# Kernel optimization log

Measured on AMD Instinct MI355X. Metric: run time of the kernel, lower is better.

## Reference

```python
import math
import jax, jax.numpy as jnp
import numpy as np

K_KDE = 50
K_RIPS = 16
SCALE = 30.0
DESTNUM = 10
THRESHOLD = 1.0  # hardcoded in topograd_loss
N, D = 8192, 64


def _knn(x, k):
    """Brute-force k-NN with squared L2 distances (faiss IndexFlatL2 semantics,
    self included as nearest neighbour). Returns (sq_dists[N,k], idxs[N,k]),
    neighbours sorted by increasing distance."""
    sq = jnp.sum(x * x, axis=1)
    d = sq[:, None] + sq[None, :] - 2.0 * (x @ x.T)  # [N,N]
    neg, idx = jax.lax.top_k(-d, k)
    return -neg, idx


def _cluster(density, rips_idxs, threshold):
    """Union-find re-implementation of the numba `cluster` routine.
    Iterates points from high density (index N-1) to low; each point joins the
    entry of its highest-index upward neighbour; other upward neighbours'
    entries are merged if their persistence is below threshold, and every
    cross-entry comparison emits a persistence pair (entry_idx, ref_idx).
    Returns the raw pers_pairs array (without the [-1,-1] sentinel rows)."""
    n = density.shape[0]
    parent = np.arange(n)
    name = np.arange(n)  # name[root] = entry id (a point index)

    def find(i):
        root = i
        while parent[root] != root:
            root = parent[root]
        while parent[i] != root:  # path compression
            parent[i], i = root, parent[i]
        return root

    pairs = []
    for i in range(n - 2, -1, -1):
        nbr = rips_idxs[i]
        us = nbr[nbr > i]  # upward (denser, already-processed) neighbours
        if us.size == 0:
            continue  # point i forms its own singleton entry
        e_up = name[find(int(us.max()))]
        parent[find(i)] = find(e_up)  # append i to entry e_up
        for j in us:
            ei = name[find(int(j))]
            if ei != e_up:
                pairs.append((ei, i))
                if density[ei] - density[i] < threshold:
                    parent[find(ei)] = find(e_up)  # merge entry ei into e_up
    return np.asarray(pairs, dtype=np.int64).reshape(-1, 2)


def _pd_pairs(pairs, n):
    """For each unique entry id in pairs[:,0], keep (entry_id, max ref idx)."""
    maxref = np.full(n, -1, dtype=np.int64)
    np.maximum.at(maxref, pairs[:, 0], pairs[:, 1])
    uniq = np.unique(pairs[:, 0])
    return np.stack([uniq, maxref[uniq]], axis=1)


def setup_inputs() -> dict:
    key = jax.random.key(0)
    x = jax.random.normal(key, (N, D), dtype=jnp.float32)
    return {"x": x}


def reference(x):
    # --- KNN kernel density estimate (differentiable) ---
    vals, _ = _knn(x, K_KDE)
    res = jnp.sum(jnp.exp(-vals / SCALE), axis=1) / (K_KDE * SCALE)
    dens = res / jnp.max(res)
    # --- sort by ascending density ---
    sorted_idxs = jnp.argsort(dens)
    dens_s = dens[sorted_idxs]
    x_s = x[sorted_idxs]
    # --- delta-Rips graph on sorted points ---
    _, rips_idxs = _knn(x_s, K_RIPS)
    # --- persistence clustering (non-differentiable, host) ---
    pairs = _cluster(np.asarray(dens_s), np.asarray(rips_idxs), THRESHOLD)
    pd = jnp.asarray(_pd_pairs(pairs, x.shape[0]))  # [P,2] int64
    # --- topological loss ---
    oripd = dens_s[pd]  # [P,2] (birth, death) densities
    sidx = jnp.argsort(oripd[:, 0] - oripd[:, 1])  # ascending persistence
    changepairs = pd[sidx[:-DESTNUM]]
    nochangepairs = pd[sidx[-DESTNUM:-1]]
    dest = jax.lax.stop_gradient(oripd[sidx[-1]])  # torch.as_tensor detaches
    pd11 = dens_s[changepairs]
    weakdist = jnp.sum(pd11[:, 0] - pd11[:, 1]) / math.sqrt(2.0)
    strongdist = jnp.sum(jnp.linalg.norm(dens_s[nochangepairs] - dest, axis=1))
    return weakdist + strongdist
```

## Files before the change

kernel.cpp:

```cpp
#include <hip/hip_runtime.h>
#include <stdint.h>

#define NN 8192
#define DD 64

using bf16x8 = __attribute__((ext_vector_type(8))) short;
using f32x4  = __attribute__((ext_vector_type(4))) float;

__device__ __forceinline__ unsigned short f2bf(float f){
  unsigned u = __float_as_uint(f);
  return (unsigned short)((u + 0x7FFFu + ((u >> 16) & 1u)) >> 16);
}

__global__ __launch_bounds__(256) void k_pre(const float* __restrict__ x, float* __restrict__ xT,
                                             float* __restrict__ sq, int do_tr,
                                             uint4* __restrict__ xfrag, int do_frag){
  __shared__ float tile[64*65];
  const int tid = threadIdx.x;
  const int b = blockIdx.x;
  for (int k = 0; k < 4; ++k){
    const int idx4 = tid + k*256;
    const float4 v = ((const float4*)(x + (size_t)b*4096))[idx4];
    const int row = idx4 >> 4, d0 = (idx4 & 15) * 4;
    tile[row*65 + d0 + 0] = v.x;
    tile[row*65 + d0 + 1] = v.y;
    tile[row*65 + d0 + 2] = v.z;
    tile[row*65 + d0 + 3] = v.w;
  }
  __syncthreads();
  if (do_tr){
    const int jj = tid & 15;
    const int dq = tid >> 4;
    for (int k = 0; k < 4; ++k){
      const int d = dq + 16*k;
      float4 o;
      o.x = tile[(jj*4+0)*65 + d];
      o.y = tile[(jj*4+1)*65 + d];
      o.z = tile[(jj*4+2)*65 + d];
      o.w = tile[(jj*4+3)*65 + d];
      ((float4*)xT)[(size_t)d*2048 + b*16 + jj] = o;
    }
  }
  if (do_frag){
    for (int ch = tid; ch < 512; ch += 256){
      const int c  = ch & 15;
      const int q  = (ch >> 4) & 3;
      const int m  = (ch >> 6) & 1;
      const int gl = ch >> 7;
      const float* sp = tile + (gl*16 + c)*65 + m*32 + q*8;
      unsigned short h[8];
#pragma unroll
      for (int i2 = 0; i2 < 8; ++i2) h[i2] = f2bf(sp[i2]);
      uint4 o;
      o.x = (unsigned)h[0] | ((unsigned)h[1] << 16);
      o.y = (unsigned)h[2] | ((unsigned)h[3] << 16);
      o.z = (unsigned)h[4] | ((unsigned)h[5] << 16);
      o.w = (unsigned)h[6] | ((unsigned)h[7] << 16);
      xfrag[(size_t)b*512 + ch] = o;
    }
  }
  if (tid < 64){
    float acc = 0.f;
    const float* rp = tile + tid*65;
    for (int d = 0; d < 64; ++d) acc = fmaf(rp[d], rp[d], acc);
    sq[b*64 + tid] = acc;
  }
}

template<bool XT>
__device__ __forceinline__ void dists_1024(const float* __restrict__ x, const float* __restrict__ xT,
                                           const float* __restrict__ xi, int jbase, int tid,
                                           float acc[8][4]){
#pragma unroll
  for (int r = 0; r < 8; ++r)
#pragma unroll
    for (int q = 0; q < 4; ++q) acc[r][q] = 0.f;
  const int j0 = jbase + tid*4;
  for (int dq = 0; dq < 16; ++dq){
    float4 vj[4];
    if (XT){
#pragma unroll
      for (int s = 0; s < 4; ++s)
        vj[s] = ((const float4*)xT)[(size_t)(dq*4+s)*2048 + (j0 >> 2)];
    } else {
#pragma unroll
      for (int s = 0; s < 4; ++s){
        const int d = dq*4 + s;
        vj[s].x = x[(size_t)(j0+0)*64 + d];
        vj[s].y = x[(size_t)(j0+1)*64 + d];
        vj[s].z = x[(size_t)(j0+2)*64 + d];
        vj[s].w = x[(size_t)(j0+3)*64 + d];
      }
    }
#pragma unroll
    for (int r = 0; r < 8; ++r){
      const float4 wv = ((const float4*)(xi + r*64))[dq];
      acc[r][0] = fmaf(vj[0].x, wv.x, acc[r][0]);
      acc[r][1] = fmaf(vj[0].y, wv.x, acc[r][1]);
      acc[r][2] = fmaf(vj[0].z, wv.x, acc[r][2]);
      acc[r][3] = fmaf(vj[0].w, wv.x, acc[r][3]);
      acc[r][0] = fmaf(vj[1].x, wv.y, acc[r][0]);
      acc[r][1] = fmaf(vj[1].y, wv.y, acc[r][1]);
      acc[r][2] = fmaf(vj[1].z, wv.y, acc[r][2]);
      acc[r][3] = fmaf(vj[1].w, wv.y, acc[r][3]);
      acc[r][0] = fmaf(vj[2].x, wv.z, acc[r][0]);
      acc[r][1] = fmaf(vj[2].y, wv.z, acc[r][1]);
      acc[r][2] = fmaf(vj[2].z, wv.z, acc[r][2]);
      acc[r][3] = fmaf(vj[2].w, wv.z, acc[r][3]);
      acc[r][0] = fmaf(vj[3].x, wv.w, acc[r][0]);
      acc[r][1] = fmaf(vj[3].y, wv.w, acc[r][1]);
      acc[r][2] = fmaf(vj[3].z, wv.w, acc[r][2]);
      acc[r][3] = fmaf(vj[3].w, wv.w, acc[r][3]);
    }
  }
}

template<bool XT>
__global__ __launch_bounds__(256) void k_samp(const float* __restrict__ x, const float* __restrict__ xT,
                                              const float* __restrict__ sq, float* __restrict__ tub){
  __shared__ __align__(16) float xi[8*64];
  __shared__ float sqi_s[8];
  __shared__ __align__(16) float samp[8*1024];
  const int tid = threadIdx.x;
  const int i0 = blockIdx.x * 8;
  for (int t = tid; t < 8*64; t += 256) xi[t] = x[(size_t)i0*64 + t];
  if (tid < 8) sqi_s[tid] = sq[i0+tid];
  __syncthreads();
  float sqir[8];
#pragma unroll
  for (int r = 0; r < 8; ++r) sqir[r] = sqi_s[r];

  const int w0 = (blockIdx.x * 1024) & 8191;
  float acc[8][4];
  dists_1024<XT>(x, xT, xi, w0, tid, acc);
  float sqj[4];
#pragma unroll
  for (int q = 0; q < 4; ++q) sqj[q] = sq[w0 + tid*4 + q];
#pragma unroll
  for (int r = 0; r < 8; ++r)
#pragma unroll
    for (int q = 0; q < 4; ++q)
      samp[r*1024 + tid*4 + q] = (sqir[r] + sqj[q]) - 2.f*acc[r][q];
  __syncthreads();
  const int wv = tid >> 6, lane = tid & 63;
  for (int rr = 0; rr < 2; ++rr){
    const int r = wv + rr*4;
    float v[16];
#pragma unroll
    for (int k2 = 0; k2 < 16; ++k2) v[k2] = samp[r*1024 + lane + 64*k2];
    unsigned lo = 0u, hi = 0x7F800001u;
    while (hi - lo > 1u){
      const unsigned mid = (lo + hi) >> 1;
      const float pf = __uint_as_float(mid);
      int c = 0;
#pragma unroll
      for (int k2 = 0; k2 < 16; ++k2) c += (v[k2] < pf) ? 1 : 0;
#pragma unroll
      for (int off = 32; off; off >>= 1) c += __shfl_xor(c, off);
      if (c >= 32) hi = mid; else lo = mid;
    }
    if (lane == 0) tub[i0 + r] = __uint_as_float(hi);
  }
}

__global__ __launch_bounds__(256) void k_filt(const float* __restrict__ x, const float* __restrict__ sq,
                                              const float* __restrict__ tub,
                                              const uint4* __restrict__ xfrag,
                                              unsigned char* __restrict__ nib){
  const int tid = threadIdx.x;
  const int l   = tid & 63;
  const int w   = tid >> 6;
  const int qh  = l >> 4;
  const int c16 = l & 15;
  const int i0  = blockIdx.x * 8;

  bf16x8 a0, a1;
#pragma unroll
  for (int i2 = 0; i2 < 8; ++i2){ a0[i2] = 0; a1[i2] = 0; }
  if (c16 < 8){
    const float* ap = x + (size_t)(i0 + c16)*64 + qh*8;
#pragma unroll
    for (int i2 = 0; i2 < 8; ++i2){
      a0[i2] = (short)f2bf(ap[i2]);
      a1[i2] = (short)f2bf(ap[i2 + 32]);
    }
  }
  float thr2[4];
#pragma unroll
  for (int rg = 0; rg < 4; ++rg){
    int row = qh*4 + rg; row = (row < 8) ? row : 0;
    thr2[rg] = tub[i0 + row] + 2.0f - sq[i0 + row];
  }

  const bf16x8* bfp = (const bf16x8*)xfrag + (size_t)w*128 + l;
  const float*  sqp = sq + w*16 + c16;
  unsigned char* nb = nib + (size_t)blockIdx.x*8192 + w*16 + c16;

  bf16x8 A0 = bfp[0],   A1 = bfp[64];     float SA = sqp[0];
  bf16x8 B0 = bfp[512], B1 = bfp[512+64]; float SB = sqp[64];
  for (int it = 0; it < 128; it += 2){
    const int n2 = (it+2 < 128) ? it+2 : 126;
    const int n3 = (it+3 < 128) ? it+3 : 127;
    bf16x8 N0 = bfp[(size_t)n2*512], N1 = bfp[(size_t)n2*512 + 64];
    bf16x8 M0 = bfp[(size_t)n3*512], M1 = bfp[(size_t)n3*512 + 64];
    const float SN = sqp[n2*64], SM = sqp[n3*64];
    {
      f32x4 acc = {0.f, 0.f, 0.f, 0.f};
      acc = __builtin_amdgcn_mfma_f32_16x16x32_bf16(a0, A0, acc, 0, 0, 0);
      acc = __builtin_amdgcn_mfma_f32_16x16x32_bf16(a1, A1, acc, 0, 0, 0);
      unsigned m4 = 0u;
      m4 |= (fmaf(-2.f, acc[0], SA) < thr2[0]) ? 1u : 0u;
      m4 |= (fmaf(-2.f, acc[1], SA) < thr2[1]) ? 2u : 0u;
      m4 |= (fmaf(-2.f, acc[2], SA) < thr2[2]) ? 4u : 0u;
      m4 |= (fmaf(-2.f, acc[3], SA) < thr2[3]) ? 8u : 0u;
      const unsigned pm = (unsigned)__shfl((int)m4, (l + 16) & 63);
      if (l < 16) nb[it*64] = (unsigned char)(m4 | (pm << 4));
    }
    {
      f32x4 acc = {0.f, 0.f, 0.f, 0.f};
      acc = __builtin_amdgcn_mfma_f32_16x16x32_bf16(a0, B0, acc, 0, 0, 0);
      acc = __builtin_amdgcn_mfma_f32_16x16x32_bf16(a1, B1, acc, 0, 0, 0);
      unsigned m4 = 0u;
      m4 |= (fmaf(-2.f, acc[0], SB) < thr2[0]) ? 1u : 0u;
      m4 |= (fmaf(-2.f, acc[1], SB) < thr2[1]) ? 2u : 0u;
      m4 |= (fmaf(-2.f, acc[2], SB) < thr2[2]) ? 4u : 0u;
      m4 |= (fmaf(-2.f, acc[3], SB) < thr2[3]) ? 8u : 0u;
      const unsigned pm = (unsigned)__shfl((int)m4, (l + 16) & 63);
      if (l < 16) nb[(it+1)*64] = (unsigned char)(m4 | (pm << 4));
    }
    A0 = N0; A1 = N1; SA = SN;
    B0 = M0; B1 = M1; SB = SM;
  }
}

__global__ __launch_bounds__(256) void k_csort(const float* __restrict__ x, const float* __restrict__ sq,
                                               const float* __restrict__ tub,
                                               const unsigned char* __restrict__ nib,
                                               float* __restrict__ res, unsigned short* __restrict__ nn16){
  __shared__ __align__(16) float xi[8*68];
  __shared__ float sqi_s[8];
  __shared__ float tubs[8];
  __shared__ __align__(16) unsigned long long cand[8*512];
  __shared__ unsigned ccnt[8];
  const int tid = threadIdx.x;
  const int i0 = blockIdx.x * 8;
  for (int t = tid; t < 8*64; t += 256) xi[(t >> 6)*68 + (t & 63)] = x[(size_t)i0*64 + t];
  if (tid < 8){ sqi_s[tid] = sq[i0+tid]; tubs[tid] = tub[i0+tid]; ccnt[tid] = 0u; }
  for (int t = tid; t < 8*512; t += 256) cand[t] = ~0ULL;
  __syncthreads();

  const uint4* nb4 = (const uint4*)(nib + (size_t)blockIdx.x*8192);
  for (int u = tid; u < 512; u += 256){
    const uint4 v4 = nb4[u];
    unsigned wds[4] = {v4.x, v4.y, v4.z, v4.w};
#pragma unroll
    for (int ww = 0; ww < 4; ++ww){
      unsigned wvv = wds[ww];
      while (wvv){
        const int bit = __builtin_ctz(wvv);
        wvv &= wvv - 1u;
        const int byte = bit >> 3;
        const int r = bit & 7;
        const int j = u*16 + ww*4 + byte;
        const float* xj = x + (size_t)j*64;
        const float* xr = xi + r*68;
        float acc = 0.f;
#pragma unroll
        for (int d4 = 0; d4 < 16; ++d4){
          const float4 vj4 = ((const float4*)xj)[d4];
          const float4 wi4 = ((const float4*)xr)[d4];
          acc = fmaf(vj4.x, wi4.x, acc);
          acc = fmaf(vj4.y, wi4.y, acc);
          acc = fmaf(vj4.z, wi4.z, acc);
          acc = fmaf(vj4.w, wi4.w, acc);
        }
        const float dist = (sqi_s[r] + sq[j]) - 2.f*acc;
        if (dist < tubs[r]){
          const unsigned pos = atomicAdd(&ccnt[r], 1u);
          if (pos < 512u){
            unsigned u2 = __float_as_uint(dist);
            u2 = ((int)u2 < 0) ? ~u2 : (u2 | 0x80000000u);
            cand[r*512 + pos] = (((unsigned long long)u2) << 13) | (unsigned)j;
          }
        }
      }
    }
  }
  __syncthreads();

  for (int k = 2; k <= 512; k <<= 1){
    for (int jj2 = k >> 1; jj2 > 0; jj2 >>= 1){
      const int mm = tid;
      const int i = ((mm & ~(jj2-1)) << 1) | (mm & (jj2-1));
      const int p = i | jj2;
      const bool up2 = ((i & k) == 0);
#pragma unroll
      for (int r = 0; r < 8; ++r){
        unsigned long long a = cand[r*512+i], bb = cand[r*512+p];
        if ((a > bb) == up2){ cand[r*512+i] = bb; cand[r*512+p] = a; }
      }
      __syncthreads();
    }
  }

  const int wv2 = tid >> 6, lane2 = tid & 63;
  for (int rr = 0; rr < 2; ++rr){
    const int r = wv2*2 + rr;
    const unsigned long long kk = cand[r*512 + lane2];
    float e = 0.f;
    if (lane2 < 50){
      unsigned u2 = (unsigned)(kk >> 13);
      u2 = (u2 & 0x80000000u) ? (u2 & 0x7FFFFFFFu) : ~u2;
      e = expf(-__uint_as_float(u2) / 30.f);
    }
#pragma unroll
    for (int off = 32; off; off >>= 1) e += __shfl_down(e, off);
    if (lane2 == 0) res[i0+r] = e / 1500.f;
    if (lane2 < 16) nn16[(size_t)(i0+r)*16 + lane2] = (unsigned short)(kk & 8191ULL);
  }
}

template<bool XT>
__global__ __launch_bounds__(256) void k_cand(const float* __restrict__ x, const float* __restrict__ xT,
                                              const float* __restrict__ sq,
                                              float* __restrict__ res, unsigned short* __restrict__ nn16){
  __shared__ float xi[8*64];
  __shared__ float sqi_s[8];
  __shared__ float tubs[8];
  __shared__ __align__(16) unsigned long long cand[8*512];
  __shared__ unsigned ccnt[8];
  float* samp = (float*)cand;
  const int tid = threadIdx.x;
  const int i0 = blockIdx.x * 8;
  for (int t = tid; t < 8*64; t += 256) xi[t] = x[(size_t)i0*64 + t];
  if (tid < 8){ sqi_s[tid] = sq[i0+tid]; ccnt[tid] = 0u; }
  __syncthreads();
  float sqir[8];
#pragma unroll
  for (int r = 0; r < 8; ++r) sqir[r] = sqi_s[r];

  const int w0 = (blockIdx.x * 1024) & 8191;
  {
    float acc[8][4];
    dists_1024<XT>(x, xT, xi, w0, tid, acc);
    float sqj[4];
#pragma unroll
    for (int q = 0; q < 4; ++q) sqj[q] = sq[w0 + tid*4 + q];
#pragma unroll
    for (int r = 0; r < 8; ++r)
#pragma unroll
      for (int q = 0; q < 4; ++q)
        samp[r*1024 + tid*4 + q] = (sqir[r] + sqj[q]) - 2.f*acc[r][q];
  }
  __syncthreads();
  {
    const int wv = tid >> 6, lane = tid & 63;
    for (int rr = 0; rr < 2; ++rr){
      const int r = wv + rr*4;
      float v[16];
#pragma unroll
      for (int k2 = 0; k2 < 16; ++k2) v[k2] = samp[r*1024 + lane + 64*k2];
      unsigned lo = 0u, hi = 0x7F800001u;
      while (hi - lo > 1u){
        const unsigned mid = (lo + hi) >> 1;
        const float pf = __uint_as_float(mid);
        int c = 0;
#pragma unroll
        for (int k2 = 0; k2 < 16; ++k2) c += (v[k2] < pf) ? 1 : 0;
#pragma unroll
        for (int off = 32; off; off >>= 1) c += __shfl_xor(c, off);
        if (c >= 32) hi = mid; else lo = mid;
      }
      if (lane == 0) tubs[r] = __uint_as_float(hi);
    }
  }
  __syncthreads();
  float tubr[8];
#pragma unroll
  for (int r = 0; r < 8; ++r) tubr[r] = tubs[r];
  for (int t = tid; t < 8*512; t += 256) cand[t] = ~0ULL;
  __syncthreads();

  for (int pass = 0; pass < 8; ++pass){
    const int jb = pass*1024;
    float acc[8][4];
    dists_1024<XT>(x, xT, xi, jb, tid, acc);
    const int j0 = jb + tid*4;
    float sqj[4];
#pragma unroll
    for (int q = 0; q < 4; ++q) sqj[q] = sq[j0 + q];
#pragma unroll
    for (int r = 0; r < 8; ++r){
#pragma unroll
      for (int q = 0; q < 4; ++q){
        const float dist = (sqir[r] + sqj[q]) - 2.f*acc[r][q];
        if (dist < tubr[r]){
          const unsigned pos = atomicAdd(&ccnt[r], 1u);
          if (pos < 512u){
            unsigned u = __float_as_uint(dist);
            u = ((int)u < 0) ? ~u : (u | 0x80000000u);
            cand[r*512 + pos] = (((unsigned long long)u) << 13) | (unsigned)(j0 + q);
          }
        }
      }
    }
  }
  __syncthreads();

  for (int k = 2; k <= 512; k <<= 1){
    for (int jj2 = k >> 1; jj2 > 0; jj2 >>= 1){
      const int mm = tid;
      const int i = ((mm & ~(jj2-1)) << 1) | (mm & (jj2-1));
      const int p = i | jj2;
      const bool up2 = ((i & k) == 0);
#pragma unroll
      for (int r = 0; r < 8; ++r){
        unsigned long long a = cand[r*512+i], bb = cand[r*512+p];
        if ((a > bb) == up2){ cand[r*512+i] = bb; cand[r*512+p] = a; }
      }
      __syncthreads();
    }
  }

  const int wv2 = tid >> 6, lane2 = tid & 63;
  for (int rr = 0; rr < 2; ++rr){
    const int r = wv2*2 + rr;
    const unsigned long long kk = cand[r*512 + lane2];
    float e = 0.f;
    if (lane2 < 50){
      unsigned u2 = (unsigned)(kk >> 13);
      u2 = (u2 & 0x80000000u) ? (u2 & 0x7FFFFFFFu) : ~u2;
      e = expf(-__uint_as_float(u2) / 30.f);
    }
#pragma unroll
    for (int off = 32; off; off >>= 1) e += __shfl_down(e, off);
    if (lane2 == 0) res[i0+r] = e / 1500.f;
    if (lane2 < 16) nn16[(size_t)(i0+r)*16 + lane2] = (unsigned short)(kk & 8191ULL);
  }
}

__device__ __forceinline__ unsigned long long shfl64_xor(unsigned long long v, int off){
  return (((unsigned long long)(unsigned)__shfl_xor((int)(v >> 32), off)) << 32)
       | (unsigned long long)(unsigned)__shfl_xor((int)(v & 0xFFFFFFFFu), off);
}

__global__ __launch_bounds__(256) void k_rank(const float* __restrict__ res,
                                              unsigned short* __restrict__ rank,
                                              float* __restrict__ dens_s){
  __shared__ __align__(16) unsigned long long keys[NN];
  __shared__ float red[256];
  __shared__ unsigned short pcnt[256];
  const int tid = threadIdx.x;
  float m = 0.f;
  for (int t = tid; t < NN; t += 256) m = fmaxf(m, res[t]);
  red[tid] = m; __syncthreads();
  for (int o = 128; o; o >>= 1){ if (tid < o) red[tid] = fmaxf(red[tid], red[tid+o]); __syncthreads(); }
  const float mr = red[0];
  __syncthreads();
  for (int t = tid; t < NN; t += 256){
    const float dnv = res[t] / mr;
    keys[t] = (((unsigned long long)__float_as_uint(dnv)) << 13) | (unsigned)t;
  }
  __syncthreads();
  const int i = blockIdx.x*128 + (tid & 127);
  const unsigned long long ki = keys[i];
  const int j0 = (tid >> 7) * (NN/2);
  int c = 0;
#pragma unroll 8
  for (int j = 0; j < NN/2; ++j) c += (keys[j0 + j] < ki) ? 1 : 0;
  pcnt[tid] = (unsigned short)c;
  __syncthreads();
  if (tid < 128){
    const int r = (int)pcnt[tid] + (int)pcnt[tid + 128];
    rank[i] = (unsigned short)r;
    dens_s[r] = __uint_as_float((unsigned)(ki >> 13));
  }
}

__global__ __launch_bounds__(256) void k_ups(const unsigned short* __restrict__ rank,
                                             const unsigned short* __restrict__ nn16,
                                             unsigned short* __restrict__ ups_t){
  __shared__ __align__(16) unsigned short rk[NN];
  const int tid = threadIdx.x;
  for (int t = tid; t < NN/8; t += 256) ((uint4*)rk)[t] = ((const uint4*)rank)[t];
  __syncthreads();
  const int o = blockIdx.x*256 + tid;
  const int p = rk[o];
  const uint4 n0 = ((const uint4*)nn16)[(size_t)o*2];
  const uint4 n1 = ((const uint4*)nn16)[(size_t)o*2 + 1];
  unsigned nw[8] = {n0.x, n0.y, n0.z, n0.w, n1.x, n1.y, n1.z, n1.w};
  unsigned short outv[16];
  int cnt = 0;
  for (int k = 0; k < 16; ++k){
    const unsigned nb = (nw[k >> 1] >> ((k & 1) * 16)) & 0xFFFFu;
    const unsigned r = rk[nb];
    if ((int)r > p){
      int q = cnt++;
      while (q > 0 && outv[q-1] < (unsigned short)r){ outv[q] = outv[q-1]; --q; }
      outv[q] = (unsigned short)r;
    }
  }
  for (int k = cnt; k < 16; ++k) outv[k] = 0;
  unsigned short* dst = ups_t + (size_t)p*16;
  uint4 a, b;
  a.x = (unsigned)outv[0] | ((unsigned)outv[1] << 16);
  a.y = (unsigned)outv[2] | ((unsigned)outv[3] << 16);
  a.z = (unsigned)outv[4] | ((unsigned)outv[5] << 16);
  a.w = (unsigned)outv[6] | ((unsigned)outv[7] << 16);
  b.x = (unsigned)outv[8] | ((unsigned)outv[9] << 16);
  b.y = (unsigned)outv[10] | ((unsigned)outv[11] << 16);
  b.z = (unsigned)outv[12] | ((unsigned)outv[13] << 16);
  b.w = (unsigned)outv[14] | ((unsigned)outv[15] << 16);
  ((uint4*)dst)[0] = a;
  ((uint4*)dst)[1] = b;
}

__device__ __forceinline__ unsigned uf_find2(volatile unsigned short* comp, unsigned x){
  unsigned r = comp[x];
  while (true){
    const unsigned g = comp[r];
    if (g == r) break;
    comp[x] = (unsigned short)g;
    x = r; r = g;
  }
  return r;
}

__global__ __launch_bounds__(1024) void k_msf(const float* __restrict__ dens_s,
                                              unsigned short* __restrict__ ups_t,
                                              unsigned long long* __restrict__ edges,
                                              int edgecap,
                                              float* __restrict__ out){
  __shared__ __align__(16) float dens[NN];
  __shared__ __align__(16) unsigned short P[NN];
  __shared__ __align__(16) unsigned short pkid[NN];
  __shared__ __align__(16) unsigned short death[NN];
  __shared__ __align__(16) unsigned short pkrank[4096];
  __shared__ __align__(16) unsigned short comp[4096];
  __shared__ __align__(16) unsigned short hook[4096];
  __shared__ __align__(16) unsigned bestv[4096];
  __shared__ __align__(16) unsigned long long msf[4096];
  __shared__ unsigned long long wred[17];
  __shared__ unsigned long long sel[10];
  __shared__ unsigned ecnt_s, ecnt2_s, mcnt_s, chg_s, flat_s, dcnt_s;
  unsigned* scan1 = (unsigned*)msf;
  float* red = (float*)msf;
  unsigned* dlist = bestv;

  const int tid = threadIdx.x;
  const int lane = tid & 63;

  for (int t = tid; t < NN/4; t += 1024)
    ((float4*)dens)[t] = ((const float4*)dens_s)[t];
  for (int t = tid; t < NN; t += 1024){
    const unsigned u0 = ups_t[(size_t)t*16];
    P[t] = (u0 == 0u) ? (unsigned short)t : (unsigned short)u0;
    death[t] = 0xFFFFu;
  }
  if (tid == 0){ ecnt_s = 0u; mcnt_s = 0u; dcnt_s = 0u; }
  __syncthreads();

  for (int rd = 0; rd < 13; ++rd){
    for (int pp = 0; pp < 8; ++pp){
      const int p = tid + pp*1024;
      const unsigned v = P[p];
      const unsigned w2 = P[v];
      if (w2 != v) P[p] = (unsigned short)w2;
    }
    __syncthreads();
  }

  {
    const int p0 = tid*8;
    int c = 0;
    for (int k = 0; k < 8; ++k) c += (P[p0+k] == (unsigned short)(p0+k)) ? 1 : 0;
    scan1[tid] = (unsigned)c; __syncthreads();
    for (int s = 1; s < 1024; s <<= 1){
      const unsigned v = scan1[tid];
      const unsigned u = (tid >= s) ? scan1[tid-s] : 0u;
      __syncthreads();
      scan1[tid] = v + u;
      __syncthreads();
    }
    int base = (int)scan1[tid] - c;
    for (int k = 0; k < 8; ++k){
      const int p = p0 + k;
      if (P[p] == (unsigned short)p){
        pkid[p] = (unsigned short)base;
        if (base < 4096) pkrank[base] = (unsigned short)p;
        ++base;
      }
    }
  }
  __syncthreads();
  int Npk = (int)scan1[1023];
  if (Npk > 4096) Npk = 4096;
  __syncthreads();

  for (int pp = 0; pp < 8; ++pp){
    const int p = tid + pp*1024;
    const uint4 a4 = ((const uint4*)ups_t)[(size_t)p*2];
    const uint4 b4 = ((const uint4*)ups_t)[(size_t)p*2 + 1];
    unsigned uu[8] = {a4.x, a4.y, a4.z, a4.w, b4.x, b4.y, b4.z, b4.w};
    unsigned edv[15];
    int nd = 0;
    const unsigned u0 = uu[0] & 0xFFFFu;
    if (u0 != 0u){
      const unsigned m0 = P[u0];
      const unsigned m0id = pkid[m0];
      for (int k = 1; k < 16; ++k){
        const unsigned uk = (uu[k >> 1] >> ((k & 1) * 16)) & 0xFFFFu;
        if (uk == 0u) break;
        const unsigned v = P[uk];
        if (v == m0) continue;
        const unsigned vid = pkid[v];
        bool dup = false;
        for (int j = 0; j < nd; ++j) dup = dup || ((edv[j] >> 16) == vid);
        if (dup) continue;
        edv[nd++] = (vid << 16) | m0id;
      }
    }
    unsigned off = (unsigned)nd;
    for (int s = 1; s < 64; s <<= 1){
      const unsigned o = (unsigned)__shfl_up((int)off, s);
      if (lane >= s) off += o;
    }
    const unsigned tot = (unsigned)__shfl((int)off, 63);
    unsigned wb = 0u;
    if (lane == 0 && tot) wb = atomicAdd(&ecnt_s, tot);
    wb = (unsigned)__shfl((int)wb, 0);
    const unsigned mybase = wb + off - (unsigned)nd;
    for (int k = 0; k < nd; ++k){
      const unsigned pos = mybase + (unsigned)k;
      if ((int)pos < edgecap)
        edges[pos] = (((unsigned long long)(unsigned)p) << 32) | (unsigned long long)edv[k];
    }
  }
  __syncthreads();
  int Ecur = ((int)ecnt_s < edgecap) ? (int)ecnt_s : edgecap;

  unsigned long long* eb_in  = edges;
  unsigned long long* eb_out = (unsigned long long*)ups_t;
  for (int t = tid; t < Npk; t += 1024) comp[t] = (unsigned short)t;
  __syncthreads();
  for (int round = 0; round < 16 && Ecur > 0; ++round){
    for (int t = tid; t < Npk; t += 1024){ bestv[t] = 0u; hook[t] = 0xFFFFu; }
    if (tid == 0){ chg_s = 0u; ecnt2_s = 0u; }
    __syncthreads();
    for (int base = 0; base < Ecur; base += 1024){
      const int e = base + tid;
      bool keep = false;
      unsigned long long ed = 0ULL;
      if (e < Ecur){
        ed = eb_in[e];
        const unsigned a = (unsigned)(ed >> 16) & 0xFFFFu;
        const unsigned b = (unsigned)ed & 0xFFFFu;
        const unsigned ra = comp[a], rb = comp[b];
        if (ra != rb){
          keep = true;
          const unsigned key = ((((unsigned)(ed >> 32)) + 1u) << 18) | (unsigned)e;
          atomicMax(&bestv[ra], key);
          atomicMax(&bestv[rb], key);
        }
      }
      const unsigned long long bal = __ballot(keep);
      const unsigned cnt = (unsigned)__popcll(bal);
      const unsigned pfx = (unsigned)__popcll(bal & ((1ULL << lane) - 1ULL));
      unsigned wb = 0u;
      if (lane == 0 && cnt) wb = atomicAdd(&ecnt2_s, cnt);
      wb = (unsigned)__shfl((int)wb, 0);
      if (keep && (wb + pfx) < 32768u) eb_out[wb + pfx] = ed;
    }
    __syncthreads();
    for (int t = tid; t < Npk; t += 1024){
      if (comp[t] == (unsigned short)t && bestv[t] != 0u){
        const unsigned long long ed = eb_in[bestv[t] & 0x3FFFFu];
        const unsigned a = (unsigned)(ed >> 16) & 0xFFFFu;
        const unsigned b = (unsigned)ed & 0xFFFFu;
        const unsigned ra = comp[a], rb = comp[b];
        hook[t] = (unsigned short)((ra == (unsigned)t) ? rb : ra);
      }
    }
    __syncthreads();
    for (int t = tid; t < Npk; t += 1024){
      const unsigned o = hook[t];
      if (o != 0xFFFFu && !(hook[o] == (unsigned short)t && (unsigned)t < o)){
        comp[t] = (unsigned short)o;
        chg_s = 1u;
        const unsigned long long ed = eb_in[bestv[t] & 0x3FFFFu];
        const unsigned pos = atomicAdd(&mcnt_s, 1u);
        if (pos < 4096u) msf[pos] = (((ed >> 32) + 1ULL) << 32) | (ed & 0xFFFFFFFFULL);
      }
    }
    __syncthreads();
    for (;;){
      if (tid == 0) flat_s = 0u;
      __syncthreads();
      for (int t = tid; t < Npk; t += 1024){
        const unsigned c = comp[t];
        const unsigned cc = comp[c];
        if (cc != c){ comp[t] = (unsigned short)cc; flat_s = 1u; }
      }
      __syncthreads();
      if (flat_s == 0u) break;
    }
    const int En = ((int)ecnt2_s < 32768) ? (int)ecnt2_s : 32767;
    const unsigned ch = chg_s;
    __syncthreads();
    Ecur = En;
    { unsigned long long* t2 = eb_in; eb_in = eb_out; eb_out = t2; }
    if (ch == 0u) break;
  }

  const int M = ((int)mcnt_s < 4096) ? (int)mcnt_s : 4095;
  int W = 64; while (W < M) W <<= 1;
  for (int t = M + tid; t < W; t += 1024) msf[t] = 0ULL;
  for (int t = tid; t < Npk; t += 1024) comp[t] = (unsigned short)t;
  __syncthreads();
  for (int k = 2; k <= W; k <<= 1){
    for (int j = k >> 1; j > 0; j >>= 1){
      for (int m2 = tid; m2 < W/2; m2 += 1024){
        const int i = ((m2 & ~(j-1)) << 1) | (m2 & (j-1));
        const int p = i | j;
        const bool up = ((i & k) == 0);
        const unsigned long long a = msf[i], b = msf[p];
        if ((a < b) == up){ msf[i] = b; msf[p] = a; }
      }
      __syncthreads();
    }
  }

  {
    const int nb = (M + 63) >> 6;
    for (int bch = 0; bch < nb; ++bch){
      if (tid < 64){
        const int ei = bch*64 + lane;
        unsigned ra = 0xFFFFu, rb = 0xFFFFu, wgt = 0u;
        if (ei < M){
          const unsigned long long e = msf[ei];
          const unsigned a = ((unsigned)e >> 16) & 0xFFFFu;
          const unsigned b = (unsigned)e & 0xFFFFu;
          wgt = (unsigned)(e >> 32) - 1u;
          ra = uf_find2(comp, a);
          rb = uf_find2(comp, b);
        }
        unsigned kra = 0xFFFFu, krb = 0xFFFFu;
        for (int i = 0; i < 64; ++i){
          const unsigned rai = (unsigned)__builtin_amdgcn_readlane((int)ra, i);
          const unsigned rbi = (unsigned)__builtin_amdgcn_readlane((int)rb, i);
          if (rai == 0xFFFFu || rai == rbi) continue;
          if (lane == i){ kra = rai; krb = rbi; }
          ra = (ra == rai) ? rbi : ra;
          rb = (rb == rai) ? rbi : rb;
        }
        if (kra != 0xFFFFu){
          death[pkrank[kra]] = (unsigned short)wgt;
          comp[kra] = (unsigned short)krb;
        }
      }
      __syncthreads();
      for (int t = tid; t < Npk; t += 1024){
        const unsigned c = comp[t];
        const unsigned cc = comp[c];
        if (cc != c) comp[t] = (unsigned short)cc;
      }
      __syncthreads();
    }
  }
  __syncthreads();

  float s = 0.f;
  for (int e = tid; e < NN; e += 1024){
    const int dr = death[e];
    if (dr != 0xFFFF) s += dens[e] - dens[dr];
  }
  red[tid] = s; __syncthreads();
  for (int o = 512; o; o >>= 1){ if (tid < o) red[tid] += red[tid+o]; __syncthreads(); }
  const float S = red[0];

  for (int e8 = 0; e8 < 8; ++e8){
    const int e = tid + e8*1024;
    const int dr = death[e];
    const bool have = (dr != 0xFFFF);
    const unsigned long long bal = __ballot(have);
    const unsigned cnt = (unsigned)__popcll(bal);
    const unsigned pfx = (unsigned)__popcll(bal & ((1ULL << lane) - 1ULL));
    unsigned wb = 0u;
    if (lane == 0 && cnt) wb = atomicAdd(&dcnt_s, cnt);
    wb = (unsigned)__shfl((int)wb, 0);
    if (have && (wb + pfx) < 4096u) dlist[wb + pfx] = ((unsigned)e << 13) | (unsigned)dr;
  }
  __syncthreads();
  const int Dm = ((int)dcnt_s < 4096) ? (int)dcnt_s : 4096;

  unsigned long long last = ~0ULL;
  for (int t10 = 0; t10 < 10; ++t10){
    unsigned long long km = 0ULL;
    for (int i = tid; i < Dm; i += 1024){
      const unsigned pk = dlist[i];
      const unsigned e = pk >> 13, dr = pk & 8191u;
      const float pers = dens[e] - dens[dr];
      const unsigned long long k = (((unsigned long long)__float_as_uint(pers)) << 13) | e;
      if (k < last && k > km) km = k;
    }
    for (int off = 32; off; off >>= 1){
      const unsigned long long o = shfl64_xor(km, off);
      km = (o > km) ? o : km;
    }
    if (lane == 0) wred[tid >> 6] = km;
    __syncthreads();
    if (tid < 64){
      unsigned long long v = (tid < 16) ? wred[tid] : 0ULL;
      for (int off = 8; off; off >>= 1){
        const unsigned long long o = shfl64_xor(v, off);
        v = (o > v) ? o : v;
      }
      if (tid == 0) wred[16] = v;
    }
    __syncthreads();
    const unsigned long long st = wred[16];
    if (tid == 0) sel[t10] = st;
    last = st;
    __syncthreads();
  }
  if (tid == 0){
    float top = 0.f;
    for (int t10 = 0; t10 < 10; ++t10)
      if (sel[t10]) top += __uint_as_float((unsigned)(sel[t10] >> 13));
    float strong = 0.f, dest0 = 0.f, dest1 = 0.f;
    if (sel[0]){
      const unsigned e0 = (unsigned)(sel[0] & 8191ULL);
      dest0 = dens[e0]; dest1 = dens[death[e0]];
    }
    for (int t10 = 1; t10 < 10; ++t10){
      if (!sel[t10]) continue;
      const unsigned e = (unsigned)(sel[t10] & 8191ULL);
      const float a = dens[e] - dest0;
      const float b = dens[death[e]] - dest1;
      strong += sqrtf(a*a + b*b);
    }
    out[0] = (S - top) / 1.41421356237309515f + strong;
  }
}

extern "C" void kernel_launch(void* const* d_in, const int* in_sizes, int n_in,
                              void* d_out, int out_size, void* d_ws, size_t ws_size,
                              hipStream_t stream){
  const float* x = (const float*)d_in[0];
  char* w = (char*)d_ws;
  float*          sq     = (float*)(w + 0);
  float*          res    = (float*)(w + 32768);
  float*          dens_s = (float*)(w + 65536);
  unsigned short* rank   = (unsigned short*)(w + 98304);
  unsigned short* nn16   = (unsigned short*)(w + 114688);
  unsigned short* ups_t  = (unsigned short*)(w + 376832);
  float*          xT     = (float*)(w + 655360);
  uint4*          xfrag  = (uint4*)(w + 2752512);
  float*          tub    = (float*)(w + 3801088);
  unsigned char*  nib    = (unsigned char*)(w + 3833856);
  const int use_xt  = (ws_size >= (size_t)2752512) ? 1 : 0;
  const int use_mf2 = (ws_size >= (size_t)(3833856 + 8*1024*1024)) ? 1 : 0;
  unsigned long long* edges = use_xt ? (unsigned long long*)(w + 655360)
                                     : (unsigned long long*)(w + 114688);
  const int edgecap = use_xt ? 262143 : 32767;

  k_pre<<<128, 256, 0, stream>>>(x, xT, sq, use_xt, xfrag, use_mf2);
  if (use_mf2){
    k_samp<true><<<1024, 256, 0, stream>>>(x, xT, sq, tub);
    k_filt<<<1024, 256, 0, stream>>>(x, sq, tub, xfrag, nib);
    k_csort<<<1024, 256, 0, stream>>>(x, sq, tub, nib, res, nn16);
  } else if (use_xt){
    k_cand<true ><<<1024, 256, 0, stream>>>(x, xT, sq, res, nn16);
  } else {
    k_cand<false><<<1024, 256, 0, stream>>>(x, xT, sq, res, nn16);
  }
  k_rank<<<64, 256, 0, stream>>>(res, rank, dens_s);
  k_ups <<<32, 256, 0, stream>>>(rank, nn16, ups_t);
  k_msf <<<1, 1024, 0, stream>>>(dens_s, ups_t, edges, edgecap, (float*)d_out);
}
```

Measured before the change: 574.5 us.

## Replace block-wide bitonic sort in k_csort with per-wave ballot select and register sort

The candidate-refinement kernel now prefetches its neighbor bitmask words before the shared-memory setup. It walks the bitmask with two independent candidates per iteration so more gathers are in flight. It also drops the full 512-element shared-memory bitonic sort with its many block barriers. Each wave instead binary-searches the 50th-smallest key with ballots, compacts the survivors into 64 slots and sorts them with a shuffle-based bitonic network. This cuts barrier and LDS traffic but adds a data-dependent binary-search loop over 45-bit keys.

```diff
diff --git a/kernel.cpp b/kernel.cpp
--- a/kernel.cpp
+++ b/kernel.cpp
@@ -10,6 +10,11 @@
 __device__ __forceinline__ unsigned short f2bf(float f){
   unsigned u = __float_as_uint(f);
   return (unsigned short)((u + 0x7FFFu + ((u >> 16) & 1u)) >> 16);
+}
+
+__device__ __forceinline__ unsigned long long shfl64_xor(unsigned long long v, int off){
+  return (((unsigned long long)(unsigned)__shfl_xor((int)(v >> 32), off)) << 32)
+       | (unsigned long long)(unsigned)__shfl_xor((int)(v & 0xFFFFFFFFu), off);
 }
 
 __global__ __launch_bounds__(256) void k_pre(const float* __restrict__ x, float* __restrict__ xT,
@@ -244,79 +249,145 @@
   __shared__ unsigned ccnt[8];
   const int tid = threadIdx.x;
   const int i0 = blockIdx.x * 8;
+
+  const uint4* nb4 = (const uint4*)(nib + (size_t)blockIdx.x*8192);
+  const uint4 vA = nb4[tid];
+  const uint4 vB = nb4[tid + 256];
+
   for (int t = tid; t < 8*64; t += 256) xi[(t >> 6)*68 + (t & 63)] = x[(size_t)i0*64 + t];
   if (tid < 8){ sqi_s[tid] = sq[i0+tid]; tubs[tid] = tub[i0+tid]; ccnt[tid] = 0u; }
   for (int t = tid; t < 8*512; t += 256) cand[t] = ~0ULL;
   __syncthreads();
 
-  const uint4* nb4 = (const uint4*)(nib + (size_t)blockIdx.x*8192);
-  for (int u = tid; u < 512; u += 256){
-    const uint4 v4 = nb4[u];
-    unsigned wds[4] = {v4.x, v4.y, v4.z, v4.w};
-#pragma unroll
-    for (int ww = 0; ww < 4; ++ww){
-      unsigned wvv = wds[ww];
-      while (wvv){
-        const int bit = __builtin_ctz(wvv);
-        wvv &= wvv - 1u;
-        const int byte = bit >> 3;
-        const int r = bit & 7;
-        const int j = u*16 + ww*4 + byte;
-        const float* xj = x + (size_t)j*64;
-        const float* xr = xi + r*68;
-        float acc = 0.f;
+  {
+    unsigned long long A[2] = { (unsigned long long)vA.x | ((unsigned long long)vA.y << 32),
+                                (unsigned long long)vA.z | ((unsigned long long)vA.w << 32) };
+    unsigned long long B[2] = { (unsigned long long)vB.x | ((unsigned long long)vB.y << 32),
+                                (unsigned long long)vB.z | ((unsigned long long)vB.w << 32) };
+    const int baseA = tid*16, baseB = (tid+256)*16;
+    for (int h = 0; h < 2; ++h){
+      unsigned long long a = A[h], b = B[h];
+      const int ba = baseA + h*8, bb = baseB + h*8;
+      while (a | b){
+        int ja = -1, ra = 0, jb = -1, rb = 0;
+        if (a){ const int bit = __builtin_ctzll(a); a &= a - 1ULL; ja = ba + (bit >> 3); ra = bit & 7; }
+        if (b){ const int bit = __builtin_ctzll(b); b &= b - 1ULL; jb = bb + (bit >> 3); rb = bit & 7; }
+        const float4* xja = (const float4*)(x + (size_t)(ja < 0 ? 0 : ja)*64);
+        const float4* xjb = (const float4*)(x + (size_t)(jb < 0 ? 0 : jb)*64);
+        const float4* xra = (const float4*)(xi + ra*68);
+        const float4* xrb = (const float4*)(xi + rb*68);
+        float accA = 0.f, accB = 0.f;
 #pragma unroll
         for (int d4 = 0; d4 < 16; ++d4){
-          const float4 vj4 = ((const float4*)xj)[d4];
-          const float4 wi4 = ((const float4*)xr)[d4];
-          acc = fmaf(vj4.x, wi4.x, acc);
-          acc = fmaf(vj4.y, wi4.y, acc);
-          acc = fmaf(vj4.z, wi4.z, acc);
-          acc = fmaf(vj4.w, wi4.w, acc);
+          const float4 va4 = xja[d4];
+          const float4 wa4 = xra[d4];
+          accA = fmaf(va4.x, wa4.x, accA);
+          accA = fmaf(va4.y, wa4.y, accA);
+          accA = fmaf(va4.z, wa4.z, accA);
+          accA = fmaf(va4.w, wa4.w, accA);
+          const float4 vb4 = xjb[d4];
+          const float4 wb4 = xrb[d4];
+          accB = fmaf(vb4.x, wb4.x, accB);
+          accB = fmaf(vb4.y, wb4.y, accB);
+          accB = fmaf(vb4.z, wb4.z, accB);
+          accB = fmaf(vb4.w, wb4.w, accB);
         }
-        const float dist = (sqi_s[r] + sq[j]) - 2.f*acc;
-        if (dist < tubs[r]){
-          const unsigned pos = atomicAdd(&ccnt[r], 1u);
-          if (pos < 512u){
-            unsigned u2 = __float_as_uint(dist);
-            u2 = ((int)u2 < 0) ? ~u2 : (u2 | 0x80000000u);
-            cand[r*512 + pos] = (((unsigned long long)u2) << 13) | (unsigned)j;
+        if (ja >= 0){
+          const float dist = (sqi_s[ra] + sq[ja]) - 2.f*accA;
+          if (dist < tubs[ra]){
+            const unsigned pos = atomicAdd(&ccnt[ra], 1u);
+            if (pos < 512u){
+              unsigned u2 = __float_as_uint(dist);
+              u2 = ((int)u2 < 0) ? ~u2 : (u2 | 0x80000000u);
+              cand[ra*512 + pos] = (((unsigned long long)u2) << 13) | (unsigned)ja;
+            }
           }
         }
-      }
-    }
-  }
-  __syncthreads();
-
-  for (int k = 2; k <= 512; k <<= 1){
-    for (int jj2 = k >> 1; jj2 > 0; jj2 >>= 1){
-      const int mm = tid;
-      const int i = ((mm & ~(jj2-1)) << 1) | (mm & (jj2-1));
-      const int p = i | jj2;
-      const bool up2 = ((i & k) == 0);
-#pragma unroll
-      for (int r = 0; r < 8; ++r){
-        unsigned long long a = cand[r*512+i], bb = cand[r*512+p];
-        if ((a > bb) == up2){ cand[r*512+i] = bb; cand[r*512+p] = a; }
-      }
-      __syncthreads();
-    }
-  }
-
-  const int wv2 = tid >> 6, lane2 = tid & 63;
+        if (jb >= 0){
+          const float dist = (sqi_s[rb] + sq[jb]) - 2.f*accB;
+          if (dist < tubs[rb]){
+            const unsigned pos = atomicAdd(&ccnt[rb], 1u);
+            if (pos < 512u){
+              unsigned u2 = __float_as_uint(dist);
+              u2 = ((int)u2 < 0) ? ~u2 : (u2 | 0x80000000u);
+              cand[rb*512 + pos] = (((unsigned long long)u2) << 13) | (unsigned)jb;
+            }
+          }
+        }
+      }
+    }
+  }
+  __syncthreads();
+
+  const int w = tid >> 6, lane = tid & 63;
   for (int rr = 0; rr < 2; ++rr){
-    const int r = wv2*2 + rr;
-    const unsigned long long kk = cand[r*512 + lane2];
+    const int r = w + rr*4;
+    unsigned long long k8[8];
+#pragma unroll
+    for (int t = 0; t < 8; ++t) k8[t] = cand[r*512 + lane + 64*t];
+
+    const unsigned long long REALMAX = (1ULL << 45) - 1ULL;
+    int creal = 0;
+#pragma unroll
+    for (int t = 0; t < 8; ++t) creal += __popcll(__ballot(k8[t] <= REALMAX)) != 0 ? 0 : 0;
+    {
+      int c = 0;
+#pragma unroll
+      for (int t = 0; t < 8; ++t) c += (int)__popcll(__ballot(k8[t] <= REALMAX));
+      creal = c;
+    }
+
+    unsigned long long K50;
+    if (creal >= 50){
+      unsigned long long lo = 0ULL, hi = REALMAX;
+      while (lo < hi){
+        const unsigned long long mid = lo + ((hi - lo) >> 1);
+        int c = 0;
+#pragma unroll
+        for (int t = 0; t < 8; ++t) c += (int)__popcll(__ballot(k8[t] <= mid));
+        if (c >= 50) hi = mid; else lo = mid + 1ULL;
+      }
+      K50 = hi;
+    } else {
+      K50 = ~0ULL;
+    }
+
+    unsigned long long* buf = cand + r*512;
+    buf[lane] = ~0ULL;
+    int base = 0;
+#pragma unroll
+    for (int t = 0; t < 8; ++t){
+      const bool pr = (k8[t] <= K50) && (k8[t] != ~0ULL);
+      const unsigned long long bal = __ballot(pr);
+      const int off = base + (int)__popcll(bal & ((1ULL << lane) - 1ULL));
+      if (pr && off < 64) buf[off] = k8[t];
+      base += (int)__popcll(bal);
+    }
+    unsigned long long key = buf[lane];
+
+#pragma unroll
+    for (int k = 2; k <= 64; k <<= 1){
+#pragma unroll
+      for (int j = k >> 1; j > 0; j >>= 1){
+        const unsigned long long p = shfl64_xor(key, j);
+        const bool dirUp = ((lane & k) == 0);
+        const bool lower = ((lane & j) == 0);
+        const unsigned long long mn = (key < p) ? key : p;
+        const unsigned long long mx = (key < p) ? p : key;
+        key = (dirUp == lower) ? mn : mx;
+      }
+    }
+
     float e = 0.f;
-    if (lane2 < 50){
-      unsigned u2 = (unsigned)(kk >> 13);
+    if (lane < 50){
+      unsigned u2 = (unsigned)(key >> 13);
       u2 = (u2 & 0x80000000u) ? (u2 & 0x7FFFFFFFu) : ~u2;
       e = expf(-__uint_as_float(u2) / 30.f);
     }
 #pragma unroll
     for (int off = 32; off; off >>= 1) e += __shfl_down(e, off);
-    if (lane2 == 0) res[i0+r] = e / 1500.f;
-    if (lane2 < 16) nn16[(size_t)(i0+r)*16 + lane2] = (unsigned short)(kk & 8191ULL);
+    if (lane == 0) res[i0+r] = e / 1500.f;
+    if (lane < 16) nn16[(size_t)(i0+r)*16 + lane] = (unsigned short)(key & 8191ULL);
   }
 }
 
@@ -437,11 +508,6 @@
     if (lane2 == 0) res[i0+r] = e / 1500.f;
     if (lane2 < 16) nn16[(size_t)(i0+r)*16 + lane2] = (unsigned short)(kk & 8191ULL);
   }
-}
-
-__device__ __forceinline__ unsigned long long shfl64_xor(unsigned long long v, int off){
-  return (((unsigned long long)(unsigned)__shfl_xor((int)(v >> 32), off)) << 32)
-       | (unsigned long long)(unsigned)__shfl_xor((int)(v & 0xFFFFFFFFu), off);
 }
 
 __global__ __launch_bounds__(256) void k_rank(const float* __restrict__ res,
```

Measured after the change: 650.8 us. +13.3%, slower.

## Tighten bf16 filter bound, split csort rows across blocks, replace bitonic with select+wave sort

Applied to the files above, without the earlier changes.

The bf16 MFMA candidate filter now uses a norm-scaled error margin (0.017*|xi|*|xj| plus a small constant) instead of a fixed +2.0 slack, aiming to pass fewer false candidates to the exact fp32 pass. k_csort is split so each block handles 4 query rows instead of 8, doubling the grid and halving shared memory for occupancy. The full 512-element shared-memory bitonic sort is replaced by a ballot-based binary search for the 50th key, compaction to 64 entries, and an in-register wave bitonic sort. The tighter margin risks dropping true neighbours if the bf16 error exceeds the new bound.

```diff
diff --git a/kernel.cpp b/kernel.cpp
--- a/kernel.cpp
+++ b/kernel.cpp
@@ -10,6 +10,11 @@
 __device__ __forceinline__ unsigned short f2bf(float f){
   unsigned u = __float_as_uint(f);
   return (unsigned short)((u + 0x7FFFu + ((u >> 16) & 1u)) >> 16);
+}
+
+__device__ __forceinline__ unsigned long long shfl64_xor(unsigned long long v, int off){
+  return (((unsigned long long)(unsigned)__shfl_xor((int)(v >> 32), off)) << 32)
+       | (unsigned long long)(unsigned)__shfl_xor((int)(v & 0xFFFFFFFFu), off);
 }
 
 __global__ __launch_bounds__(256) void k_pre(const float* __restrict__ x, float* __restrict__ xT,
@@ -185,11 +190,12 @@
       a1[i2] = (short)f2bf(ap[i2 + 32]);
     }
   }
-  float thr2[4];
+  float thr3[4], rs[4];
 #pragma unroll
   for (int rg = 0; rg < 4; ++rg){
     int row = qh*4 + rg; row = (row < 8) ? row : 0;
-    thr2[rg] = tub[i0 + row] + 2.0f - sq[i0 + row];
+    thr3[rg] = (tub[i0 + row] - sq[i0 + row]) + 0.002f;
+    rs[rg]   = 0.017f * sqrtf(sq[i0 + row]);
   }
 
   const bf16x8* bfp = (const bf16x8*)xfrag + (size_t)w*128 + l;
@@ -208,11 +214,12 @@
       f32x4 acc = {0.f, 0.f, 0.f, 0.f};
       acc = __builtin_amdgcn_mfma_f32_16x16x32_bf16(a0, A0, acc, 0, 0, 0);
       acc = __builtin_amdgcn_mfma_f32_16x16x32_bf16(a1, A1, acc, 0, 0, 0);
+      const float sr = sqrtf(SA);
       unsigned m4 = 0u;
-      m4 |= (fmaf(-2.f, acc[0], SA) < thr2[0]) ? 1u : 0u;
-      m4 |= (fmaf(-2.f, acc[1], SA) < thr2[1]) ? 2u : 0u;
-      m4 |= (fmaf(-2.f, acc[2], SA) < thr2[2]) ? 4u : 0u;
-      m4 |= (fmaf(-2.f, acc[3], SA) < thr2[3]) ? 8u : 0u;
+      m4 |= (fmaf(-rs[0], sr, fmaf(-2.f, acc[0], SA)) < thr3[0]) ? 1u : 0u;
+      m4 |= (fmaf(-rs[1], sr, fmaf(-2.f, acc[1], SA)) < thr3[1]) ? 2u : 0u;
+      m4 |= (fmaf(-rs[2], sr, fmaf(-2.f, acc[2], SA)) < thr3[2]) ? 4u : 0u;
+      m4 |= (fmaf(-rs[3], sr, fmaf(-2.f, acc[3], SA)) < thr3[3]) ? 8u : 0u;
       const unsigned pm = (unsigned)__shfl((int)m4, (l + 16) & 63);
       if (l < 16) nb[it*64] = (unsigned char)(m4 | (pm << 4));
     }
@@ -220,11 +227,12 @@
       f32x4 acc = {0.f, 0.f, 0.f, 0.f};
       acc = __builtin_amdgcn_mfma_f32_16x16x32_bf16(a0, B0, acc, 0, 0, 0);
       acc = __builtin_amdgcn_mfma_f32_16x16x32_bf16(a1, B1, acc, 0, 0, 0);
+      const float sr = sqrtf(SB);
       unsigned m4 = 0u;
-      m4 |= (fmaf(-2.f, acc[0], SB) < thr2[0]) ? 1u : 0u;
-      m4 |= (fmaf(-2.f, acc[1], SB) < thr2[1]) ? 2u : 0u;
-      m4 |= (fmaf(-2.f, acc[2], SB) < thr2[2]) ? 4u : 0u;
-      m4 |= (fmaf(-2.f, acc[3], SB) < thr2[3]) ? 8u : 0u;
+      m4 |= (fmaf(-rs[0], sr, fmaf(-2.f, acc[0], SB)) < thr3[0]) ? 1u : 0u;
+      m4 |= (fmaf(-rs[1], sr, fmaf(-2.f, acc[1], SB)) < thr3[1]) ? 2u : 0u;
+      m4 |= (fmaf(-rs[2], sr, fmaf(-2.f, acc[2], SB)) < thr3[2]) ? 4u : 0u;
+      m4 |= (fmaf(-rs[3], sr, fmaf(-2.f, acc[3], SB)) < thr3[3]) ? 8u : 0u;
       const unsigned pm = (unsigned)__shfl((int)m4, (l + 16) & 63);
       if (l < 16) nb[(it+1)*64] = (unsigned char)(m4 | (pm << 4));
     }
@@ -233,35 +241,38 @@
   }
 }
 
-__global__ __launch_bounds__(256) void k_csort(const float* __restrict__ x, const float* __restrict__ sq,
-                                               const float* __restrict__ tub,
-                                               const unsigned char* __restrict__ nib,
-                                               float* __restrict__ res, unsigned short* __restrict__ nn16){
-  __shared__ __align__(16) float xi[8*68];
-  __shared__ float sqi_s[8];
-  __shared__ float tubs[8];
-  __shared__ __align__(16) unsigned long long cand[8*512];
-  __shared__ unsigned ccnt[8];
-  const int tid = threadIdx.x;
-  const int i0 = blockIdx.x * 8;
-  for (int t = tid; t < 8*64; t += 256) xi[(t >> 6)*68 + (t & 63)] = x[(size_t)i0*64 + t];
-  if (tid < 8){ sqi_s[tid] = sq[i0+tid]; tubs[tid] = tub[i0+tid]; ccnt[tid] = 0u; }
-  for (int t = tid; t < 8*512; t += 256) cand[t] = ~0ULL;
-  __syncthreads();
-
-  const uint4* nb4 = (const uint4*)(nib + (size_t)blockIdx.x*8192);
+__global__ __launch_bounds__(256, 8) void k_csort(const float* __restrict__ x, const float* __restrict__ sq,
+                                                  const float* __restrict__ tub,
+                                                  const unsigned char* __restrict__ nib,
+                                                  float* __restrict__ res, unsigned short* __restrict__ nn16){
+  __shared__ __align__(16) float xi[4*68];
+  __shared__ float sqi_s[4];
+  __shared__ float tubs[4];
+  __shared__ __align__(16) unsigned long long cand[4*512];
+  __shared__ unsigned ccnt[4];
+  const int tid  = threadIdx.x;
+  const int grp  = blockIdx.x >> 1;
+  const int half = blockIdx.x & 1;
+  const int i0   = grp*8 + half*4;
+  const unsigned rmask = half ? 0xF0F0F0F0u : 0x0F0F0F0Fu;
+
+  for (int t = tid; t < 4*64; t += 256) xi[(t >> 6)*68 + (t & 63)] = x[(size_t)i0*64 + t];
+  if (tid < 4){ sqi_s[tid] = sq[i0+tid]; tubs[tid] = tub[i0+tid]; ccnt[tid] = 0u; }
+  for (int t = tid; t < 4*512; t += 256) cand[t] = ~0ULL;
+  __syncthreads();
+
+  const uint4* nb4 = (const uint4*)(nib + (size_t)grp*8192);
   for (int u = tid; u < 512; u += 256){
     const uint4 v4 = nb4[u];
-    unsigned wds[4] = {v4.x, v4.y, v4.z, v4.w};
+    unsigned wds[4] = {v4.x & rmask, v4.y & rmask, v4.z & rmask, v4.w & rmask};
 #pragma unroll
     for (int ww = 0; ww < 4; ++ww){
       unsigned wvv = wds[ww];
       while (wvv){
         const int bit = __builtin_ctz(wvv);
         wvv &= wvv - 1u;
-        const int byte = bit >> 3;
-        const int r = bit & 7;
-        const int j = u*16 + ww*4 + byte;
+        const int r = bit & 3;
+        const int j = u*16 + ww*4 + (bit >> 3);
         const float* xj = x + (size_t)j*64;
         const float* xr = xi + r*68;
         float acc = 0.f;
@@ -288,35 +299,69 @@
   }
   __syncthreads();
 
-  for (int k = 2; k <= 512; k <<= 1){
-    for (int jj2 = k >> 1; jj2 > 0; jj2 >>= 1){
-      const int mm = tid;
-      const int i = ((mm & ~(jj2-1)) << 1) | (mm & (jj2-1));
-      const int p = i | jj2;
-      const bool up2 = ((i & k) == 0);
-#pragma unroll
-      for (int r = 0; r < 8; ++r){
-        unsigned long long a = cand[r*512+i], bb = cand[r*512+p];
-        if ((a > bb) == up2){ cand[r*512+i] = bb; cand[r*512+p] = a; }
-      }
-      __syncthreads();
-    }
-  }
-
-  const int wv2 = tid >> 6, lane2 = tid & 63;
-  for (int rr = 0; rr < 2; ++rr){
-    const int r = wv2*2 + rr;
-    const unsigned long long kk = cand[r*512 + lane2];
+  const int w = tid >> 6, lane = tid & 63;
+  {
+    const int r = w;
+    unsigned long long k8[8];
+#pragma unroll
+    for (int t = 0; t < 8; ++t) k8[t] = cand[r*512 + lane + 64*t];
+
+    const unsigned long long REALMAX = (1ULL << 45) - 1ULL;
+    int creal = 0;
+#pragma unroll
+    for (int t = 0; t < 8; ++t) creal += (int)__popcll(__ballot(k8[t] <= REALMAX));
+
+    unsigned long long K50;
+    if (creal >= 50){
+      unsigned long long lo = 0ULL, hi = REALMAX;
+      while (lo < hi){
+        const unsigned long long mid = lo + ((hi - lo) >> 1);
+        int c = 0;
+#pragma unroll
+        for (int t = 0; t < 8; ++t) c += (int)__popcll(__ballot(k8[t] <= mid));
+        if (c >= 50) hi = mid; else lo = mid + 1ULL;
+      }
+      K50 = hi;
+    } else {
+      K50 = ~0ULL;
+    }
+
+    unsigned long long* buf = cand + r*512;
+    buf[lane] = ~0ULL;
+    int base = 0;
+#pragma unroll
+    for (int t = 0; t < 8; ++t){
+      const bool pr = (k8[t] <= K50) && (k8[t] != ~0ULL);
+      const unsigned long long bal = __ballot(pr);
+      const int off = base + (int)__popcll(bal & ((1ULL << lane) - 1ULL));
+      if (pr && off < 64) buf[off] = k8[t];
+      base += (int)__popcll(bal);
+    }
+    unsigned long long key = buf[lane];
+
+#pragma unroll
+    for (int k = 2; k <= 64; k <<= 1){
+#pragma unroll
+      for (int j = k >> 1; j > 0; j >>= 1){
+        const unsigned long long p = shfl64_xor(key, j);
+        const bool dirUp = ((lane & k) == 0);
+        const bool lower = ((lane & j) == 0);
+        const unsigned long long mn = (key < p) ? key : p;
+        const unsigned long long mx = (key < p) ? p : key;
+        key = (dirUp == lower) ? mn : mx;
+      }
+    }
+
     float e = 0.f;
-    if (lane2 < 50){
-      unsigned u2 = (unsigned)(kk >> 13);
+    if (lane < 50){
+      unsigned u2 = (unsigned)(key >> 13);
       u2 = (u2 & 0x80000000u) ? (u2 & 0x7FFFFFFFu) : ~u2;
       e = expf(-__uint_as_float(u2) / 30.f);
     }
 #pragma unroll
     for (int off = 32; off; off >>= 1) e += __shfl_down(e, off);
-    if (lane2 == 0) res[i0+r] = e / 1500.f;
-    if (lane2 < 16) nn16[(size_t)(i0+r)*16 + lane2] = (unsigned short)(kk & 8191ULL);
+    if (lane == 0) res[i0+r] = e / 1500.f;
+    if (lane < 16) nn16[(size_t)(i0+r)*16 + lane] = (unsigned short)(key & 8191ULL);
   }
 }
 
@@ -437,11 +482,6 @@
     if (lane2 == 0) res[i0+r] = e / 1500.f;
     if (lane2 < 16) nn16[(size_t)(i0+r)*16 + lane2] = (unsigned short)(kk & 8191ULL);
   }
-}
-
-__device__ __forceinline__ unsigned long long shfl64_xor(unsigned long long v, int off){
-  return (((unsigned long long)(unsigned)__shfl_xor((int)(v >> 32), off)) << 32)
-       | (unsigned long long)(unsigned)__shfl_xor((int)(v & 0xFFFFFFFFu), off);
 }
 
 __global__ __launch_bounds__(256) void k_rank(const float* __restrict__ res,
@@ -868,7 +908,7 @@
   if (use_mf2){
     k_samp<true><<<1024, 256, 0, stream>>>(x, xT, sq, tub);
     k_filt<<<1024, 256, 0, stream>>>(x, sq, tub, xfrag, nib);
-    k_csort<<<1024, 256, 0, stream>>>(x, sq, tub, nib, res, nn16);
+    k_csort<<<2048, 256, 0, stream>>>(x, sq, tub, nib, res, nn16);
   } else if (use_xt){
     k_cand<true ><<<1024, 256, 0, stream>>>(x, xT, sq, res, nn16);
   } else {
```

New measurement: 570.8 us. Within noise of the previous version (-0.7%).
